# Kernel optimization log

Measured on AMD Instinct MI355X. Metric: run time of the kernel, lower is better.

## Reference

```python
import jax, jax.numpy as jnp
import numpy as np

N_AGENTS = 16
OBS_DIM = 256
ACT_DIM = 32
B, T = 16, 64
ADAPTIVE = max(10, N_AGENTS)  # 16 Monte-Carlo counterfactual samples
H1, H2 = 128, 64


def setup_inputs() -> dict:
    key = jax.random.key(0)
    ks = jax.random.split(key, 10)
    in_dim = OBS_DIM + ACT_DIM
    inp = {
        "obs": jax.random.normal(ks[0], (B, T, N_AGENTS, OBS_DIM), dtype=jnp.float32),
        "actions": jax.random.uniform(ks[1], (B, T, N_AGENTS, ACT_DIM), dtype=jnp.float32),
        "cf_actions": jax.random.uniform(ks[2], (N_AGENTS, ADAPTIVE, B, T, ACT_DIM), dtype=jnp.float32),
        "W1": jax.random.normal(ks[3], (in_dim, H1), dtype=jnp.float32) / np.sqrt(in_dim),
        "b1": jnp.zeros((H1,), dtype=jnp.float32),
        "W2": jax.random.normal(ks[4], (H1, H2), dtype=jnp.float32) / np.sqrt(H1),
        "b2": jnp.zeros((H2,), dtype=jnp.float32),
        "W3": jax.random.normal(ks[5], (H2, ACT_DIM), dtype=jnp.float32) / np.sqrt(H2),
        "b3": jnp.zeros((ACT_DIM,), dtype=jnp.float32),
    }
    return inp


def _mlp(x, W1, b1, W2, b2, W3, b3):
    h = jax.nn.relu(x @ W1 + b1)
    h = jax.nn.relu(h @ W2 + b2)
    return h @ W3 + b3


def reference(obs, actions, cf_actions, W1, b1, W2, b2, W3, b3):
    # obs: [B,T,N,D], actions: [B,T,N,A], cf_actions: [N,S,B,T,A]
    obs_n = jnp.moveaxis(obs, 2, 0)      # [N,B,T,D]
    act_n = jnp.moveaxis(actions, 2, 0)  # [N,B,T,A]

    # p(with k): MLP([obs_k, action_k]) for all agents at once  -> [N,B,T,A]
    p_with = _mlp(jnp.concatenate([obs_n, act_n], axis=-1), W1, b1, W2, b2, W3, b3)
    # p(zero action)
    p_zero = _mlp(jnp.concatenate([obs_n, jnp.zeros_like(act_n)], axis=-1),
                  W1, b1, W2, b2, W3, b3)
    # Monte-Carlo counterfactuals: [N,S,B,T,A]
    S = cf_actions.shape[1]
    obs_rep = jnp.broadcast_to(obs_n[:, None], (obs_n.shape[0], S) + obs_n.shape[1:])
    p_cf = _mlp(jnp.concatenate([obs_rep, cf_actions], axis=-1), W1, b1, W2, b2, W3, b3)

    p_without = (p_zero + p_cf.sum(axis=1)) / (S + 1)  # [N,B,T,A]

    # F.kl_div(log_softmax(p_with), softmax(p_without), reduction='none')
    log_p = jax.nn.log_softmax(p_with, axis=-1)
    q = jax.nn.softmax(p_without, axis=-1)
    log_q = jax.nn.log_softmax(p_without, axis=-1)
    kl = q * (log_q - log_p)  # [N,B,T,A]

    # stack over agents on last dim then mean over action dim -> [B,T,N]
    influences = jnp.moveaxis(kl.mean(axis=-1), 0, -1)
    return influences
```

## Files before the change

### kernel.cpp

```cpp
#include <hip/hip_runtime.h>

#define NAG   16
#define OBSD  256
#define ACTD  32
#define SCF   16
#define H1D   128
#define H2D   64
#define BT    1024
#define NTOK  16384
#define NEVAL 18

typedef float f4 __attribute__((ext_vector_type(4)));

#define OBS_OFF  0
#define BS_OFF   8192
#define W1S_OFF  0
#define W2S_OFF  4096
#define HS_OFF   12288
#define H2S_OFF  16384
#define LDS_FLOATS 18432

#define X1(r) (((r) & 7) << 2)
#define X2(r) (((r) & 7) << 3)

__global__ __launch_bounds__(256, 2) void k_fused(
    const float* __restrict__ obs, const float* __restrict__ actions,
    const float* __restrict__ cf, const float* __restrict__ W1,
    const float* __restrict__ b1, const float* __restrict__ W2,
    const float* __restrict__ b2v, const float* __restrict__ W3,
    const float* __restrict__ b3v, float* __restrict__ out)
{
    __shared__ float lds[LDS_FLOATS];

    const int tid = threadIdx.x;
    const int g0  = blockIdx.x * 32;

    const int rb1 = tid >> 5, cb1 = tid & 31;
    const int kh = tid >> 7;
    const int rg = (tid >> 4) & 7;
    const int cg = tid & 15;
    const int r3 = tid >> 3, cb3 = tid & 7;

    {
        const float* src = obs + g0 * OBSD;
        #pragma unroll
        for (int j = 0; j < 8; ++j) {
            int idx = tid + j * 256;
            *(f4*)(lds + OBS_OFF + idx * 4) = *(const f4*)(src + idx * 4);
        }
    }

    float acc[4][4] = {};
    for (int kt = 0; kt < OBSD; kt += 32) {
        __syncthreads();
        const float* wsrc = W1 + kt * H1D;
        #pragma unroll
        for (int u = 0; u < 4; ++u)
            *(f4*)(lds + BS_OFF + u * 1024 + tid * 4) =
                *(const f4*)(wsrc + u * 1024 + tid * 4);
        __syncthreads();
        #pragma unroll
        for (int k0 = 0; k0 < 32; k0 += 4) {
            f4 a[4], b[4];
            #pragma unroll
            for (int i = 0; i < 4; ++i)
                a[i] = *(const f4*)(lds + OBS_OFF + (rb1 * 4 + i) * OBSD + kt + k0);
            #pragma unroll
            for (int kk = 0; kk < 4; ++kk)
                b[kk] = *(const f4*)(lds + BS_OFF + (k0 + kk) * H1D + cb1 * 4);
            #pragma unroll
            for (int i = 0; i < 4; ++i)
                #pragma unroll
                for (int kk = 0; kk < 4; ++kk)
                    #pragma unroll
                    for (int j = 0; j < 4; ++j)
                        acc[i][j] = fmaf(a[i][kk], b[kk][j], acc[i][j]);
        }
    }
    f4 hobs[4];
    {
        f4 bias = *(const f4*)(b1 + cb1 * 4);
        #pragma unroll
        for (int i = 0; i < 4; ++i)
            #pragma unroll
            for (int j = 0; j < 4; ++j)
                hobs[i][j] = acc[i][j] + bias[j];
    }
    __syncthreads();

    #pragma unroll
    for (int u = 0; u < 4; ++u)
        *(f4*)(lds + W1S_OFF + u * 1024 + tid * 4) =
            *(const f4*)(W1 + OBSD * H1D + u * 1024 + tid * 4);
    #pragma unroll
    for (int u = 0; u < 8; ++u)
        *(f4*)(lds + W2S_OFF + u * 1024 + tid * 4) =
            *(const f4*)(W2 + u * 1024 + tid * 4);

    f4 bias2 = *(const f4*)(b2v + cg * 4);
    f4 bias3 = *(const f4*)(b3v + cb3 * 4);

    const int row0 = rb1 * 4;
    const int n0   = row0 & 15;
    const int btt  = (g0 >> 4) + (row0 >> 4);

    f4 pw = {0.f, 0.f, 0.f, 0.f};
    f4 pq = {0.f, 0.f, 0.f, 0.f};

    __syncthreads();

    for (int e = 0; e < NEVAL; ++e) {
        f4 hv[4];
        if (e != 1) {
            const float* asrc;
            int astride;
            if (e == 0) { asrc = actions + (g0 + row0) * ACTD; astride = ACTD; }
            else {
                asrc = cf + n0 * (SCF * BT * ACTD) + (e - 2) * (BT * ACTD)
                          + btt * ACTD;
                astride = SCF * BT * ACTD;
            }
            float a1c[4][4] = {};
            #pragma unroll
            for (int k0 = 0; k0 < ACTD; k0 += 4) {
                f4 a[4], b[4];
                #pragma unroll
                for (int i = 0; i < 4; ++i)
                    a[i] = *(const f4*)(asrc + i * astride + k0);
                #pragma unroll
                for (int kk = 0; kk < 4; ++kk)
                    b[kk] = *(const f4*)(lds + W1S_OFF + (k0 + kk) * H1D + cb1 * 4);
                #pragma unroll
                for (int i = 0; i < 4; ++i)
                    #pragma unroll
                    for (int kk = 0; kk < 4; ++kk)
                        #pragma unroll
                        for (int j = 0; j < 4; ++j)
                            a1c[i][j] = fmaf(a[i][kk], b[kk][j], a1c[i][j]);
            }
            #pragma unroll
            for (int i = 0; i < 4; ++i)
                #pragma unroll
                for (int j = 0; j < 4; ++j)
                    hv[i][j] = fmaxf(hobs[i][j] + a1c[i][j], 0.f);
        } else {
            #pragma unroll
            for (int i = 0; i < 4; ++i)
                #pragma unroll
                for (int j = 0; j < 4; ++j)
                    hv[i][j] = fmaxf(hobs[i][j], 0.f);
        }
        #pragma unroll
        for (int i = 0; i < 4; ++i) {
            int r = rb1 * 4 + i;
            *(f4*)(lds + HS_OFF + r * H1D + ((cb1 * 4) ^ X1(r))) = hv[i];
        }
        __syncthreads();

        float acc2[4][4] = {};
        {
            const int kb = kh * 64;
            #pragma unroll 8
            for (int k0 = 0; k0 < 64; k0 += 4) {
                f4 a[4], b[4];
                #pragma unroll
                for (int i = 0; i < 4; ++i) {
                    int r = rg * 4 + i;
                    a[i] = *(const f4*)(lds + HS_OFF + r * H1D + ((kb + k0) ^ X1(r)));
                }
                #pragma unroll
                for (int kk = 0; kk < 4; ++kk)
                    b[kk] = *(const f4*)(lds + W2S_OFF + (kb + k0 + kk) * H2D + cg * 4);
                #pragma unroll
                for (int i = 0; i < 4; ++i)
                    #pragma unroll
                    for (int kk = 0; kk < 4; ++kk)
                        #pragma unroll
                        for (int j = 0; j < 4; ++j)
                            acc2[i][j] = fmaf(a[i][kk], b[kk][j], acc2[i][j]);
            }
        }
        if (kh) {
            #pragma unroll
            for (int i = 0; i < 4; ++i) {
                int r = rg * 4 + i;
                f4 v = {acc2[i][0], acc2[i][1], acc2[i][2], acc2[i][3]};
                *(f4*)(lds + H2S_OFF + r * H2D + ((cg * 4) ^ X2(r))) = v;
            }
        }
        __syncthreads();
        if (!kh) {
            #pragma unroll
            for (int i = 0; i < 4; ++i) {
                int r = rg * 4 + i;
                float* p = lds + H2S_OFF + r * H2D + ((cg * 4) ^ X2(r));
                f4 part = *(const f4*)p;
                f4 v;
                #pragma unroll
                for (int j = 0; j < 4; ++j)
                    v[j] = fmaxf(acc2[i][j] + part[j] + bias2[j], 0.f);
                *(f4*)p = v;
            }
        }
        __syncthreads();

        {
            f4 a3 = {0.f, 0.f, 0.f, 0.f};
            #pragma unroll 8
            for (int k0 = 0; k0 < H2D; k0 += 4) {
                f4 a = *(const f4*)(lds + H2S_OFF + r3 * H2D + (k0 ^ X2(r3)));
                #pragma unroll
                for (int kk = 0; kk < 4; ++kk) {
                    f4 b = *(const f4*)(W3 + (k0 + kk) * ACTD + cb3 * 4);
                    #pragma unroll
                    for (int j = 0; j < 4; ++j)
                        a3[j] = fmaf(a[kk], b[j], a3[j]);
                }
            }
            #pragma unroll
            for (int j = 0; j < 4; ++j) a3[j] += bias3[j];
            if (e == 0) pw = a3;
            else {
                #pragma unroll
                for (int j = 0; j < 4; ++j) pq[j] += a3[j];
            }
        }
        __syncthreads();
    }

    const float inv17 = 1.0f / 17.0f;
    f4 qv;
    #pragma unroll
    for (int j = 0; j < 4; ++j) qv[j] = pq[j] * inv17;

    float mw = fmaxf(fmaxf(pw[0], pw[1]), fmaxf(pw[2], pw[3]));
    float mq = fmaxf(fmaxf(qv[0], qv[1]), fmaxf(qv[2], qv[3]));
    #pragma unroll
    for (int m = 1; m < 8; m <<= 1) {
        mw = fmaxf(mw, __shfl_xor(mw, m));
        mq = fmaxf(mq, __shfl_xor(mq, m));
    }
    float sw = 0.f, sq = 0.f;
    #pragma unroll
    for (int j = 0; j < 4; ++j) {
        sw += expf(pw[j] - mw);
        sq += expf(qv[j] - mq);
    }
    #pragma unroll
    for (int m = 1; m < 8; m <<= 1) {
        sw += __shfl_xor(sw, m);
        sq += __shfl_xor(sq, m);
    }
    const float lsw = logf(sw), lsq = logf(sq);
    float kl = 0.f;
    #pragma unroll
    for (int j = 0; j < 4; ++j) {
        float lq = qv[j] - mq - lsq;
        float lp = pw[j] - mw - lsw;
        kl += expf(lq) * (lq - lp);
    }
    #pragma unroll
    for (int m = 1; m < 8; m <<= 1) kl += __shfl_xor(kl, m);

    if (cb3 == 0) out[g0 + r3] = kl * (1.0f / 32.0f);
}

extern "C" void kernel_launch(void* const* d_in, const int* in_sizes, int n_in,
                              void* d_out, int out_size, void* d_ws, size_t ws_size,
                              hipStream_t stream)
{
    const float* obs     = (const float*)d_in[0];
    const float* actions = (const float*)d_in[1];
    const float* cf      = (const float*)d_in[2];
    const float* W1      = (const float*)d_in[3];
    const float* b1      = (const float*)d_in[4];
    const float* W2      = (const float*)d_in[5];
    const float* b2      = (const float*)d_in[6];
    const float* W3      = (const float*)d_in[7];
    const float* b3      = (const float*)d_in[8];
    float* outp = (float*)d_out;

    k_fused<<<NTOK / 32, 256, 0, stream>>>(obs, actions, cf, W1, b1, W2,
                                           b2, W3, b3, outp);
}
```

Baseline: 264.1 us.

## Split the 18 MLP evaluations across two 256-thread teams per block

Doubles the block to 512 threads organised as two teams. Each team runs 9 of the 18 evaluations (with, zero, counterfactuals) using its own hidden-activation LDS buffers, and the partial counterfactual sums are combined through LDS before the KL step. The obs projection is now computed by all 512 threads and passed through LDS. The action-slice W1 rows are read from global memory instead of being staged in LDS. The aim is to halve the serial evaluation chain per block and raise occupancy, at the cost of more LDS per block, more register pressure under the 512x4 launch bound, and uncached W1 reads.

Result: slower. 453.1 us (+71.5%).

```diff
diff --git a/kernel.cpp b/kernel.cpp
--- a/kernel.cpp
+++ b/kernel.cpp
@@ -12,18 +12,17 @@
 
 typedef float f4 __attribute__((ext_vector_type(4)));
 
-#define OBS_OFF  0
-#define BS_OFF   8192
-#define W1S_OFF  0
-#define W2S_OFF  4096
-#define HS_OFF   12288
+#define W2S_OFF  0
+#define HS_OFF   8192
 #define H2S_OFF  16384
-#define LDS_FLOATS 18432
+#define OBS_OFF  8192
+#define BS_OFF   16384
+#define LDS_FLOATS 20480
 
 #define X1(r) (((r) & 7) << 2)
 #define X2(r) (((r) & 7) << 3)
 
-__global__ __launch_bounds__(256, 2) void k_fused(
+__global__ __launch_bounds__(512, 4) void k_fused(
     const float* __restrict__ obs, const float* __restrict__ actions,
     const float* __restrict__ cf, const float* __restrict__ W1,
     const float* __restrict__ b1, const float* __restrict__ W2,
@@ -32,111 +31,103 @@
 {
     __shared__ float lds[LDS_FLOATS];
 
-    const int tid = threadIdx.x;
-    const int g0  = blockIdx.x * 32;
-
-    const int rb1 = tid >> 5, cb1 = tid & 31;
-    const int kh = tid >> 7;
-    const int rg = (tid >> 4) & 7;
-    const int cg = tid & 15;
-    const int r3 = tid >> 3, cb3 = tid & 7;
-
+    const int tid  = threadIdx.x;
+    const int team = tid >> 8;
+    const int ttid = tid & 255;
+    const int g0   = blockIdx.x * 32;
+
+    const int rp = tid >> 5;
+    const int cp = tid & 31;
+    const int rb1 = ttid >> 5, cb1 = ttid & 31;
+    const int kh  = ttid >> 7;
+    const int rg  = (ttid >> 4) & 7, cg = ttid & 15;
+    const int r3  = ttid >> 3, cb3 = ttid & 7;
+
+    #pragma unroll
+    for (int j = 0; j < 4; ++j) {
+        int idx = tid + j * 512;
+        *(f4*)(lds + W2S_OFF + idx * 4) = *(const f4*)(W2 + idx * 4);
+        *(f4*)(lds + OBS_OFF + idx * 4) = *(const f4*)(obs + g0 * OBSD + idx * 4);
+    }
+    __syncthreads();
+
+    f4 pacc[2] = {{0.f,0.f,0.f,0.f},{0.f,0.f,0.f,0.f}};
+    for (int kt = 0; kt < OBSD; kt += 32) {
+        #pragma unroll
+        for (int j = 0; j < 2; ++j) {
+            int idx = tid + j * 512;
+            *(f4*)(lds + BS_OFF + idx * 4) = *(const f4*)(W1 + kt * H1D + idx * 4);
+        }
+        __syncthreads();
+        #pragma unroll
+        for (int k0 = 0; k0 < 32; k0 += 4) {
+            f4 a0 = *(const f4*)(lds + OBS_OFF + (rp * 2 + 0) * OBSD + kt + k0);
+            f4 a1 = *(const f4*)(lds + OBS_OFF + (rp * 2 + 1) * OBSD + kt + k0);
+            #pragma unroll
+            for (int kk = 0; kk < 4; ++kk) {
+                f4 b = *(const f4*)(lds + BS_OFF + (k0 + kk) * H1D + cp * 4);
+                pacc[0] += b * a0[kk];
+                pacc[1] += b * a1[kk];
+            }
+        }
+        __syncthreads();
+    }
     {
-        const float* src = obs + g0 * OBSD;
-        #pragma unroll
-        for (int j = 0; j < 8; ++j) {
-            int idx = tid + j * 256;
-            *(f4*)(lds + OBS_OFF + idx * 4) = *(const f4*)(src + idx * 4);
-        }
-    }
-
-    float acc[4][4] = {};
-    for (int kt = 0; kt < OBSD; kt += 32) {
-        __syncthreads();
-        const float* wsrc = W1 + kt * H1D;
-        #pragma unroll
-        for (int u = 0; u < 4; ++u)
-            *(f4*)(lds + BS_OFF + u * 1024 + tid * 4) =
-                *(const f4*)(wsrc + u * 1024 + tid * 4);
-        __syncthreads();
-        #pragma unroll
-        for (int k0 = 0; k0 < 32; k0 += 4) {
-            f4 a[4], b[4];
-            #pragma unroll
-            for (int i = 0; i < 4; ++i)
-                a[i] = *(const f4*)(lds + OBS_OFF + (rb1 * 4 + i) * OBSD + kt + k0);
-            #pragma unroll
-            for (int kk = 0; kk < 4; ++kk)
-                b[kk] = *(const f4*)(lds + BS_OFF + (k0 + kk) * H1D + cb1 * 4);
-            #pragma unroll
-            for (int i = 0; i < 4; ++i)
-                #pragma unroll
-                for (int kk = 0; kk < 4; ++kk)
-                    #pragma unroll
-                    for (int j = 0; j < 4; ++j)
-                        acc[i][j] = fmaf(a[i][kk], b[kk][j], acc[i][j]);
-        }
-    }
+        f4 bias = *(const f4*)(b1 + cp * 4);
+        *(f4*)(lds + BS_OFF + (rp * 2 + 0) * H1D + cp * 4) = pacc[0] + bias;
+        *(f4*)(lds + BS_OFF + (rp * 2 + 1) * H1D + cp * 4) = pacc[1] + bias;
+    }
+    __syncthreads();
     f4 hobs[4];
-    {
-        f4 bias = *(const f4*)(b1 + cb1 * 4);
-        #pragma unroll
-        for (int i = 0; i < 4; ++i)
-            #pragma unroll
-            for (int j = 0; j < 4; ++j)
-                hobs[i][j] = acc[i][j] + bias[j];
-    }
-    __syncthreads();
-
     #pragma unroll
-    for (int u = 0; u < 4; ++u)
-        *(f4*)(lds + W1S_OFF + u * 1024 + tid * 4) =
-            *(const f4*)(W1 + OBSD * H1D + u * 1024 + tid * 4);
-    #pragma unroll
-    for (int u = 0; u < 8; ++u)
-        *(f4*)(lds + W2S_OFF + u * 1024 + tid * 4) =
-            *(const f4*)(W2 + u * 1024 + tid * 4);
-
+    for (int i = 0; i < 4; ++i)
+        hobs[i] = *(const f4*)(lds + BS_OFF + (rb1 * 4 + i) * H1D + cb1 * 4);
+    __syncthreads();
+
+    const float* W1a = W1 + OBSD * H1D;
     f4 bias2 = *(const f4*)(b2v + cg * 4);
     f4 bias3 = *(const f4*)(b3v + cb3 * 4);
 
     const int row0 = rb1 * 4;
-    const int n0   = row0 & 15;
-    const int btt  = (g0 >> 4) + (row0 >> 4);
+    const float* act_src = actions + (g0 + row0) * ACTD;
+    const float* cf_base = cf + (row0 & 15) * (SCF * BT * ACTD)
+                              + ((g0 >> 4) + (row0 >> 4)) * ACTD;
+
+    const int hsT  = HS_OFF  + team * 4096;
+    const int h2sT = H2S_OFF + team * 2048;
 
     f4 pw = {0.f, 0.f, 0.f, 0.f};
     f4 pq = {0.f, 0.f, 0.f, 0.f};
 
-    __syncthreads();
-
-    for (int e = 0; e < NEVAL; ++e) {
+    for (int ee = 0; ee < 9; ++ee) {
+        const bool zeroEval = (team == 1) && (ee == 0);
+        const bool withEval = (team == 0) && (ee == 0);
+
         f4 hv[4];
-        if (e != 1) {
+        if (!zeroEval) {
             const float* asrc;
-            int astride;
-            if (e == 0) { asrc = actions + (g0 + row0) * ACTD; astride = ACTD; }
+            int astr;
+            if (withEval) { asrc = act_src; astr = ACTD; }
             else {
-                asrc = cf + n0 * (SCF * BT * ACTD) + (e - 2) * (BT * ACTD)
-                          + btt * ACTD;
-                astride = SCF * BT * ACTD;
-            }
-            float a1c[4][4] = {};
+                int s = ee - 1 + team * 8;
+                asrc = cf_base + s * (BT * ACTD);
+                astr = SCF * BT * ACTD;
+            }
+            f4 a1c[4] = {{0.f,0.f,0.f,0.f},{0.f,0.f,0.f,0.f},
+                         {0.f,0.f,0.f,0.f},{0.f,0.f,0.f,0.f}};
             #pragma unroll
             for (int k0 = 0; k0 < ACTD; k0 += 4) {
-                f4 a[4], b[4];
+                f4 a[4];
                 #pragma unroll
                 for (int i = 0; i < 4; ++i)
-                    a[i] = *(const f4*)(asrc + i * astride + k0);
-                #pragma unroll
-                for (int kk = 0; kk < 4; ++kk)
-                    b[kk] = *(const f4*)(lds + W1S_OFF + (k0 + kk) * H1D + cb1 * 4);
-                #pragma unroll
-                for (int i = 0; i < 4; ++i)
+                    a[i] = *(const f4*)(asrc + i * astr + k0);
+                #pragma unroll
+                for (int kk = 0; kk < 4; ++kk) {
+                    f4 b = *(const f4*)(W1a + (k0 + kk) * H1D + cb1 * 4);
                     #pragma unroll
-                    for (int kk = 0; kk < 4; ++kk)
-                        #pragma unroll
-                        for (int j = 0; j < 4; ++j)
-                            a1c[i][j] = fmaf(a[i][kk], b[kk][j], a1c[i][j]);
+                    for (int i = 0; i < 4; ++i)
+                        a1c[i] += b * a[i][kk];
+                }
             }
             #pragma unroll
             for (int i = 0; i < 4; ++i)
@@ -153,39 +144,36 @@
         #pragma unroll
         for (int i = 0; i < 4; ++i) {
             int r = rb1 * 4 + i;
-            *(f4*)(lds + HS_OFF + r * H1D + ((cb1 * 4) ^ X1(r))) = hv[i];
-        }
-        __syncthreads();
-
-        float acc2[4][4] = {};
+            *(f4*)(lds + hsT + r * H1D + ((cb1 * 4) ^ X1(r))) = hv[i];
+        }
+        __syncthreads();
+
+        f4 acc2[4] = {{0.f,0.f,0.f,0.f},{0.f,0.f,0.f,0.f},
+                      {0.f,0.f,0.f,0.f},{0.f,0.f,0.f,0.f}};
         {
             const int kb = kh * 64;
             #pragma unroll 8
             for (int k0 = 0; k0 < 64; k0 += 4) {
-                f4 a[4], b[4];
+                f4 a[4];
                 #pragma unroll
                 for (int i = 0; i < 4; ++i) {
                     int r = rg * 4 + i;
-                    a[i] = *(const f4*)(lds + HS_OFF + r * H1D + ((kb + k0) ^ X1(r)));
-                }
-                #pragma unroll
-                for (int kk = 0; kk < 4; ++kk)
-                    b[kk] = *(const f4*)(lds + W2S_OFF + (kb + k0 + kk) * H2D + cg * 4);
-                #pragma unroll
-                for (int i = 0; i < 4; ++i)
+                    a[i] = *(const f4*)(lds + hsT + r * H1D + ((kb + k0) ^ X1(r)));
+                }
+                #pragma unroll
+                for (int kk = 0; kk < 4; ++kk) {
+                    f4 b = *(const f4*)(lds + W2S_OFF + (kb + k0 + kk) * H2D + cg * 4);
                     #pragma unroll
-                    for (int kk = 0; kk < 4; ++kk)
-                        #pragma unroll
-                        for (int j = 0; j < 4; ++j)
-                            acc2[i][j] = fmaf(a[i][kk], b[kk][j], acc2[i][j]);
+                    for (int i = 0; i < 4; ++i)
+                        acc2[i] += b * a[i][kk];
+                }
             }
         }
         if (kh) {
             #pragma unroll
             for (int i = 0; i < 4; ++i) {
                 int r = rg * 4 + i;
-                f4 v = {acc2[i][0], acc2[i][1], acc2[i][2], acc2[i][3]};
-                *(f4*)(lds + H2S_OFF + r * H2D + ((cg * 4) ^ X2(r))) = v;
+                *(f4*)(lds + h2sT + r * H2D + ((cg * 4) ^ X2(r))) = acc2[i];
             }
         }
         __syncthreads();
@@ -193,7 +181,7 @@
             #pragma unroll
             for (int i = 0; i < 4; ++i) {
                 int r = rg * 4 + i;
-                float* p = lds + H2S_OFF + r * H2D + ((cg * 4) ^ X2(r));
+                float* p = lds + h2sT + r * H2D + ((cg * 4) ^ X2(r));
                 f4 part = *(const f4*)p;
                 f4 v;
                 #pragma unroll
@@ -208,61 +196,64 @@
             f4 a3 = {0.f, 0.f, 0.f, 0.f};
             #pragma unroll 8
             for (int k0 = 0; k0 < H2D; k0 += 4) {
-                f4 a = *(const f4*)(lds + H2S_OFF + r3 * H2D + (k0 ^ X2(r3)));
+                f4 a = *(const f4*)(lds + h2sT + r3 * H2D + (k0 ^ X2(r3)));
                 #pragma unroll
                 for (int kk = 0; kk < 4; ++kk) {
                     f4 b = *(const f4*)(W3 + (k0 + kk) * ACTD + cb3 * 4);
-                    #pragma unroll
-                    for (int j = 0; j < 4; ++j)
-                        a3[j] = fmaf(a[kk], b[j], a3[j]);
-                }
-            }
-            #pragma unroll
-            for (int j = 0; j < 4; ++j) a3[j] += bias3[j];
-            if (e == 0) pw = a3;
+                    a3 += b * a[kk];
+                }
+            }
+            a3 += bias3;
+            if (withEval) pw = a3;
             else {
-                #pragma unroll
-                for (int j = 0; j < 4; ++j) pq[j] += a3[j];
-            }
-        }
-        __syncthreads();
-    }
-
-    const float inv17 = 1.0f / 17.0f;
-    f4 qv;
-    #pragma unroll
-    for (int j = 0; j < 4; ++j) qv[j] = pq[j] * inv17;
-
-    float mw = fmaxf(fmaxf(pw[0], pw[1]), fmaxf(pw[2], pw[3]));
-    float mq = fmaxf(fmaxf(qv[0], qv[1]), fmaxf(qv[2], qv[3]));
-    #pragma unroll
-    for (int m = 1; m < 8; m <<= 1) {
-        mw = fmaxf(mw, __shfl_xor(mw, m));
-        mq = fmaxf(mq, __shfl_xor(mq, m));
-    }
-    float sw = 0.f, sq = 0.f;
-    #pragma unroll
-    for (int j = 0; j < 4; ++j) {
-        sw += expf(pw[j] - mw);
-        sq += expf(qv[j] - mq);
-    }
-    #pragma unroll
-    for (int m = 1; m < 8; m <<= 1) {
-        sw += __shfl_xor(sw, m);
-        sq += __shfl_xor(sq, m);
-    }
-    const float lsw = logf(sw), lsq = logf(sq);
-    float kl = 0.f;
-    #pragma unroll
-    for (int j = 0; j < 4; ++j) {
-        float lq = qv[j] - mq - lsq;
-        float lp = pw[j] - mw - lsw;
-        kl += expf(lq) * (lq - lp);
-    }
-    #pragma unroll
-    for (int m = 1; m < 8; m <<= 1) kl += __shfl_xor(kl, m);
-
-    if (cb3 == 0) out[g0 + r3] = kl * (1.0f / 32.0f);
+                pq += a3;
+            }
+        }
+        __syncthreads();
+    }
+
+    if (team) {
+        *(f4*)(lds + HS_OFF + 4096 + r3 * 32 + cb3 * 4) = pq;
+    }
+    __syncthreads();
+    if (!team) {
+        f4 pq1 = *(const f4*)(lds + HS_OFF + 4096 + r3 * 32 + cb3 * 4);
+        const float inv17 = 1.0f / 17.0f;
+        f4 qv;
+        #pragma unroll
+        for (int j = 0; j < 4; ++j) qv[j] = (pq[j] + pq1[j]) * inv17;
+
+        float mw = fmaxf(fmaxf(pw[0], pw[1]), fmaxf(pw[2], pw[3]));
+        float mq = fmaxf(fmaxf(qv[0], qv[1]), fmaxf(qv[2], qv[3]));
+        #pragma unroll
+        for (int m = 1; m < 8; m <<= 1) {
+            mw = fmaxf(mw, __shfl_xor(mw, m));
+            mq = fmaxf(mq, __shfl_xor(mq, m));
+        }
+        float sw = 0.f, sq = 0.f;
+        #pragma unroll
+        for (int j = 0; j < 4; ++j) {
+            sw += expf(pw[j] - mw);
+            sq += expf(qv[j] - mq);
+        }
+        #pragma unroll
+        for (int m = 1; m < 8; m <<= 1) {
+            sw += __shfl_xor(sw, m);
+            sq += __shfl_xor(sq, m);
+        }
+        const float lsw = logf(sw), lsq = logf(sq);
+        float kl = 0.f;
+        #pragma unroll
+        for (int j = 0; j < 4; ++j) {
+            float lq = qv[j] - mq - lsq;
+            float lp = pw[j] - mw - lsw;
+            kl += expf(lq) * (lq - lp);
+        }
+        #pragma unroll
+        for (int m = 1; m < 8; m <<= 1) kl += __shfl_xor(kl, m);
+
+        if (cb3 == 0) out[g0 + r3] = kl * (1.0f / 32.0f);
+    }
 }
 
 extern "C" void kernel_launch(void* const* d_in, const int* in_sizes, int n_in,
@@ -280,6 +271,6 @@
     const float* b3      = (const float*)d_in[8];
     float* outp = (float*)d_out;
 
-    k_fused<<<NTOK / 32, 256, 0, stream>>>(obs, actions, cf, W1, b1, W2,
+    k_fused<<<NTOK / 32, 512, 0, stream>>>(obs, actions, cf, W1, b1, W2,
                                            b2, W3, b3, outp);
 }
```
